# Kernel tuning notes

Measured on AMD Instinct MI355X. Metric: run time of the kernel, lower is better.

The kernel has to match this reference:

```python
import jax, jax.numpy as jnp
import numpy as np
from jax import lax

LEVEL_W = 512   # nodes per tree level (also = number of trees / batch_size)
DEPTH = 16      # tree depth
N = LEVEL_W * DEPTH
DIN = 512       # inputs_dim
H = 512         # hidden_dim
E = 200         # embed_dim (GloVe)
C = 150         # num classes


def setup_inputs() -> dict:
    key = jax.random.key(0)
    ks = jax.random.split(key, 8)
    features = jax.random.normal(ks[0], (N, DIN), jnp.float32)
    embed_table = jax.random.normal(ks[1], (C + 1, E), jnp.float32) * 0.1
    Wx = jax.random.normal(ks[2], (DIN + E, 4 * H), jnp.float32) / np.sqrt(DIN + E)
    Wh = jax.random.normal(ks[3], (H, 4 * H), jnp.float32) / np.sqrt(H)
    b = jnp.zeros((4 * H,), jnp.float32)
    out_W = jax.random.normal(ks[4], (H, C), jnp.float32) / np.sqrt(H)
    out_b = jnp.zeros((C,), jnp.float32)
    keep = 0.8  # dropout = 0.2 -> shared dropout mask, scaled by 1/keep
    dropout_mask = (jax.random.bernoulli(ks[5], keep, (H,)).astype(jnp.float32) / keep)
    # forest topology: level 0 nodes are roots (parent -1); level l node's parent
    # is a random node in level l-1 (parents always processed before children)
    rng = np.random.default_rng(0)
    parent = np.full((N,), -1, dtype=np.int32)
    for l in range(1, DEPTH):
        parent[l * LEVEL_W:(l + 1) * LEVEL_W] = rng.integers((l - 1) * LEVEL_W, l * LEVEL_W, LEVEL_W)
    order = rng.permutation(N).astype(np.int32)
    return {
        "features": features, "embed_table": embed_table,
        "Wx": Wx, "Wh": Wh, "b": b, "out_W": out_W, "out_b": out_b,
        "dropout_mask": dropout_mask,
        "parent_idx": jnp.asarray(parent), "order": jnp.asarray(order),
        "batch_size": LEVEL_W,
    }


def reference(features, embed_table, Wx, Wh, b, out_W, out_b, dropout_mask,
              parent_idx, order, batch_size):
    n, din = features.shape
    h_dim = Wh.shape[0]
    n_cls = out_W.shape[1]
    depth = n // LEVEL_W

    def cell(x, h, c):
        g = x @ Wx + h @ Wh + b
        i, f, gg, o = jnp.split(g, 4, axis=-1)
        c2 = jax.nn.sigmoid(f) * c + jax.nn.sigmoid(i) * jnp.tanh(gg)
        h2 = jax.nn.sigmoid(o) * jnp.tanh(c2)
        return h2, c2

    def step(carry, l):
        h_all, c_all, cm_all, d_all = carry
        off = l * LEVEL_W
        p = lax.dynamic_slice(parent_idx, (off,), (LEVEL_W,))
        root = p < 0
        pp = jnp.where(root, 0, p)
        h_par = jnp.where(root[:, None], 0.0, h_all[pp])
        c_par = jnp.where(root[:, None], 0.0, c_all[pp])
        # roots get the 'start' embedding (row 0); others embed parent's
        # committed (argmax) label shifted by 1
        eidx = jnp.where(root, 0, cm_all[pp] + 1)
        x = jnp.concatenate(
            [lax.dynamic_slice(features, (off, 0), (LEVEL_W, din)),
             embed_table[eidx]], axis=-1)
        h, c = cell(x, h_par, c_par)
        h = h * dropout_mask
        dist = h @ out_W + out_b
        cm = jnp.argmax(dist, axis=-1).astype(jnp.int32)
        carry = (lax.dynamic_update_slice(h_all, h, (off, 0)),
                 lax.dynamic_update_slice(c_all, c, (off, 0)),
                 lax.dynamic_update_slice(cm_all, cm, (off,)),
                 lax.dynamic_update_slice(d_all, dist, (off, 0)))
        return carry, None

    init = (jnp.zeros((n, h_dim), features.dtype),
            jnp.zeros((n, h_dim), features.dtype),
            jnp.zeros((n,), jnp.int32),
            jnp.zeros((n, n_cls), features.dtype))
    (h_all, c_all, cm_all, d_all), _ = lax.scan(step, init, jnp.arange(depth))
    # reorder from processing order back to node order, drop root entries
    out_dists = d_all[order][:-batch_size]
    out_commitments = cm_all[order][:-batch_size]
    return out_dists, out_commitments
```

## Files before the change

### kernel.cpp

```cpp
#include <hip/hip_runtime.h>
#include <math.h>

#define LEVEL_W 512
#define DEPTH   16
#define NNODES  8192
#define DIN     512
#define HD      512
#define ED      200
#define NC      150
#define GDIM    2048
#define OUTROWS 7680
#define KH      512
#define KW      1024
#define NKC     16

typedef __attribute__((ext_vector_type(8))) short s8v;
typedef __attribute__((ext_vector_type(4))) float f4v;

__device__ __forceinline__ unsigned short f2bf(float x) {
    unsigned int u = __float_as_uint(x);
    u += 0x7FFFu + ((u >> 16) & 1u);
    return (unsigned short)(u >> 16);
}
__device__ __forceinline__ float bf2f(unsigned short b) {
    return __uint_as_float(((unsigned int)b) << 16);
}
__device__ __forceinline__ float sigm(float x) { return 1.0f / (1.0f + expf(-x)); }

__device__ __forceinline__ void gl_lds16(const void* g, void* l) {
    __builtin_amdgcn_global_load_lds((const __attribute__((address_space(1))) void*)g,
                                     (__attribute__((address_space(3))) void*)l, 16, 0, 0);
}

__global__ __launch_bounds__(256) void prep_w(
    const float* __restrict__ Wx, const float* __restrict__ Wh,
    unsigned short* __restrict__ w_hi, unsigned short* __restrict__ w_lo)
{
    __shared__ float Wt[64][65];
    const int t   = threadIdx.x;
    const int b   = blockIdx.x;
    const int mat = b >> 5;
    const int ns  = b & 31;
    const float* src = mat ? Wx : Wh;

    for (int kw = 0; kw < 8; ++kw) {
        __syncthreads();
        #pragma unroll
        for (int p = 0; p < 16; ++p) {
            int gl  = p >> 2;
            int kk  = (p & 3) * 16 + (t >> 4);
            int col = gl * 512 + ns * 16 + (t & 15);
            Wt[kk][gl * 16 + (t & 15)] = src[(size_t)(kw * 64 + kk) * GDIM + col];
        }
        __syncthreads();
        {
            int nl  = t >> 2;
            int cp  = t & 3;
            int nsg = ns * 64 + nl;
            int key = nsg & 7;
            __align__(16) unsigned short hv[16], lv[16];
            #pragma unroll
            for (int e = 0; e < 16; ++e) {
                float x = Wt[cp * 16 + e][nl];
                unsigned short h = f2bf(x);
                hv[e] = h;
                lv[e] = f2bf(x - bf2f(h));
            }
            size_t base = (size_t)nsg * KW + mat * 512 + kw * 64;
            int c0 = cp * 2, c1 = cp * 2 + 1;
            *(uint4*)&w_hi[base + ((c0 ^ key) * 8)] = *(const uint4*)&hv[0];
            *(uint4*)&w_hi[base + ((c1 ^ key) * 8)] = *(const uint4*)&hv[8];
            *(uint4*)&w_lo[base + ((c0 ^ key) * 8)] = *(const uint4*)&lv[0];
            *(uint4*)&w_lo[base + ((c1 ^ key) * 8)] = *(const uint4*)&lv[8];
        }
    }
}

__global__ __launch_bounds__(256) void prep_feat(
    const float* __restrict__ features, const int* __restrict__ order,
    unsigned short* __restrict__ f_hi, unsigned short* __restrict__ f_lo,
    int* __restrict__ inv)
{
    int i = blockIdx.x * 256 + threadIdx.x;
    {
        int r  = i >> 5;
        int k0 = (i & 31) * 16;
        const float* srcp = features + (size_t)r * DIN + k0;
        __align__(16) unsigned short hv[16], lv[16];
        #pragma unroll
        for (int e = 0; e < 16; ++e) {
            float x = srcp[e];
            unsigned short h = f2bf(x);
            hv[e] = h;
            lv[e] = f2bf(x - bf2f(h));
        }
        int key = r & 7;
        int c0  = (k0 >> 3) & 7;
        size_t base = (size_t)r * KH + (k0 & ~63);
        *(uint4*)&f_hi[base + ((c0 ^ key) * 8)]       = *(const uint4*)&hv[0];
        *(uint4*)&f_hi[base + (((c0 + 1) ^ key) * 8)] = *(const uint4*)&hv[8];
        *(uint4*)&f_lo[base + ((c0 ^ key) * 8)]       = *(const uint4*)&lv[0];
        *(uint4*)&f_lo[base + (((c0 + 1) ^ key) * 8)] = *(const uint4*)&lv[8];
    }
    if (i < NNODES) inv[order[i]] = i;
}

__global__ __launch_bounds__(128) void prep_embed(
    const float* __restrict__ embed, const float* __restrict__ Wx,
    const float* __restrict__ bvec, float* __restrict__ g_embed)
{
    int e    = blockIdx.y;
    int np   = blockIdx.x * 128 + threadIdx.x;
    int gate = (np >> 4) & 3, hcs = np >> 6, hcl = np & 15;
    int col  = gate * 512 + hcs * 16 + hcl;
    float acc = bvec[col];
    const float* er = embed + (size_t)e * ED;
    for (int k = 0; k < ED; ++k)
        acc += er[k] * Wx[(size_t)(DIN + k) * GDIM + col];
    g_embed[(size_t)e * GDIM + np] = acc;
}

__global__ __launch_bounds__(128) void gemm_h_cell(
    float* h_all, float* c_all,
    const int* __restrict__ parent, const int* __restrict__ cm_all,
    const unsigned short* __restrict__ w_hi, const unsigned short* __restrict__ w_lo,
    const unsigned short* __restrict__ f_hi, const unsigned short* __restrict__ f_lo,
    const float* __restrict__ g_embed, const float* __restrict__ dropout, int off)
{
    __shared__ unsigned short Ah[32 * 64], Al[32 * 64], Bh[64 * 64], Bl[64 * 64];
    __shared__ int p_s[32], rt_s[32], ei_s[32];
    const int t = threadIdx.x, w = t >> 6, lane = t & 63;
    const int ns = blockIdx.x, mt = blockIdx.y;
    const int grow0 = off + mt * 32;

    if (t < 32) {
        int p  = parent[grow0 + t];
        int rt = (p < 0) ? 1 : 0;
        p_s[t]  = rt ? 0 : p;
        rt_s[t] = rt;
        ei_s[t] = rt ? 0 : (cm_all[rt ? 0 : p] + 1);
    }
    __syncthreads();

    f4v acc[4];
    #pragma unroll
    for (int i = 0; i < 4; ++i) acc[i] = (f4v){0.f, 0.f, 0.f, 0.f};

    const int ar  = t >> 2;
    const int aq  = t & 3;
    const int ap  = p_s[ar];
    const int art = rt_s[ar];
    const float* asrc = h_all + (size_t)ap * HD + aq * 16;
    const int akey = ar & 7;
    const int ac0  = aq * 2;

    for (int kc = 0; kc < NKC; ++kc) {
        if (kc < 8) {
            float x[16];
            if (art) {
                #pragma unroll
                for (int e = 0; e < 16; ++e) x[e] = 0.f;
            } else {
                const float4* s4 = (const float4*)(asrc + kc * 64);
                float4 v0 = s4[0], v1 = s4[1], v2 = s4[2], v3 = s4[3];
                x[0] = v0.x; x[1] = v0.y; x[2] = v0.z; x[3] = v0.w;
                x[4] = v1.x; x[5] = v1.y; x[6] = v1.z; x[7] = v1.w;
                x[8] = v2.x; x[9] = v2.y; x[10] = v2.z; x[11] = v2.w;
                x[12] = v3.x; x[13] = v3.y; x[14] = v3.z; x[15] = v3.w;
            }
            __align__(16) unsigned short hv[16], lv[16];
            #pragma unroll
            for (int e = 0; e < 16; ++e) {
                unsigned short h = f2bf(x[e]);
                hv[e] = h;
                lv[e] = f2bf(x[e] - bf2f(h));
            }
            *(uint4*)&Ah[ar * 64 + ((ac0 ^ akey) * 8)]       = *(const uint4*)&hv[0];
            *(uint4*)&Ah[ar * 64 + (((ac0 + 1) ^ akey) * 8)] = *(const uint4*)&hv[8];
            *(uint4*)&Al[ar * 64 + ((ac0 ^ akey) * 8)]       = *(const uint4*)&lv[0];
            *(uint4*)&Al[ar * 64 + (((ac0 + 1) ^ akey) * 8)] = *(const uint4*)&lv[8];
        } else {
            #pragma unroll
            for (int q = 0; q < 2; ++q) {
                int ia  = w * 2 + q;
                int row = ia * 8 + (lane >> 3);
                size_t aoff = ((size_t)(grow0 + row) * KH + (kc - 8) * 64) * 2
                              + (lane & 7) * 16;
                gl_lds16((const char*)f_hi + aoff, (char*)Ah + ia * 1024);
                gl_lds16((const char*)f_lo + aoff, (char*)Al + ia * 1024);
            }
        }
        #pragma unroll
        for (int q = 0; q < 4; ++q) {
            int ib  = w * 4 + q;
            int row = ib * 8 + (lane >> 3);
            size_t boff = ((size_t)(ns * 64 + row) * KW + kc * 64) * 2
                          + (lane & 7) * 16;
            gl_lds16((const char*)w_hi + boff, (char*)Bh + ib * 1024);
            gl_lds16((const char*)w_lo + boff, (char*)Bl + ib * 1024);
        }
        __syncthreads();
        #pragma unroll
        for (int s = 0; s < 2; ++s) {
            int arow = w * 16 + (lane & 15);
            int ach  = s * 4 + (lane >> 4);
            s8v ahv = *(const s8v*)&Ah[arow * 64 + ((ach ^ (arow & 7)) * 8)];
            s8v alv = *(const s8v*)&Al[arow * 64 + ((ach ^ (arow & 7)) * 8)];
            #pragma unroll
            for (int fn = 0; fn < 4; ++fn) {
                int brow = fn * 16 + (lane & 15);
                s8v bhv = *(const s8v*)&Bh[brow * 64 + ((ach ^ (brow & 7)) * 8)];
                s8v blv = *(const s8v*)&Bl[brow * 64 + ((ach ^ (brow & 7)) * 8)];
                acc[fn] = __builtin_amdgcn_mfma_f32_16x16x32_bf16(ahv, bhv, acc[fn], 0, 0, 0);
                acc[fn] = __builtin_amdgcn_mfma_f32_16x16x32_bf16(ahv, blv, acc[fn], 0, 0, 0);
                acc[fn] = __builtin_amdgcn_mfma_f32_16x16x32_bf16(alv, bhv, acc[fn], 0, 0, 0);
            }
        }
        __syncthreads();
    }

    const int hcl  = lane & 15;
    const int hcol = ns * 16 + hcl;
    const float dm = dropout[hcol];
    #pragma unroll
    for (int j = 0; j < 4; ++j) {
        int lr   = w * 16 + (lane >> 4) * 4 + j;
        int grow = grow0 + lr;
        const float* gep = g_embed + (size_t)ei_s[lr] * GDIM + ns * 64;
        float gi = acc[0][j] + gep[0 * 16 + hcl];
        float gf = acc[1][j] + gep[1 * 16 + hcl];
        float gg = acc[2][j] + gep[2 * 16 + hcl];
        float go = acc[3][j] + gep[3 * 16 + hcl];
        float cpar = rt_s[lr] ? 0.f : c_all[(size_t)p_s[lr] * HD + hcol];
        float c2 = sigm(gf) * cpar + sigm(gi) * tanhf(gg);
        float h2 = sigm(go) * tanhf(c2) * dm;
        c_all[(size_t)grow * HD + hcol] = c2;
        h_all[(size_t)grow * HD + hcol] = h2;
    }
}

__global__ __launch_bounds__(256) void level_dist(
    const float* __restrict__ h_all, const float* __restrict__ outW,
    const float* __restrict__ outb, const int* __restrict__ inv,
    float* __restrict__ d_out, int* __restrict__ cm_all, int off)
{
    __shared__ float h_s[4][512];
    __shared__ float dist_s[4][160];

    const int tid = threadIdx.x;
    const int r0  = blockIdx.x * 4;

    for (int i4 = tid; i4 < 512; i4 += 256) {
        int row = i4 >> 7;
        int k   = (i4 & 127) * 4;
        *(float4*)&h_s[row][k] =
            *(const float4*)&h_all[(size_t)(off + r0 + row) * HD + k];
    }
    __syncthreads();

    const int j = tid;
    if (j < NC) {
        float a0 = 0.f, a1 = 0.f, a2 = 0.f, a3 = 0.f;
        for (int k = 0; k < HD; ++k) {
            float w = outW[k * NC + j];
            a0 += h_s[0][k] * w;
            a1 += h_s[1][k] * w;
            a2 += h_s[2][k] * w;
            a3 += h_s[3][k] * w;
        }
        float bj = outb[j];
        dist_s[0][j] = a0 + bj;
        dist_s[1][j] = a1 + bj;
        dist_s[2][j] = a2 + bj;
        dist_s[3][j] = a3 + bj;
    }
    __syncthreads();

    if (j < NC) {
        #pragma unroll
        for (int r = 0; r < 4; ++r) {
            int orow = inv[off + r0 + r];
            if (orow < OUTROWS) d_out[(size_t)orow * NC + j] = dist_s[r][j];
        }
    }

    const int r    = tid >> 6;
    const int lane = tid & 63;
    float best = -3.402823466e38f;
    int   bidx = 0x7fffffff;
    for (int jj = lane; jj < NC; jj += 64) {
        float v = dist_s[r][jj];
        if (v > best || (v == best && jj < bidx)) { best = v; bidx = jj; }
    }
    #pragma unroll
    for (int m = 32; m >= 1; m >>= 1) {
        float ov = __shfl_xor(best, m);
        int   oi = __shfl_xor(bidx, m);
        if (ov > best || (ov == best && oi < bidx)) { best = ov; bidx = oi; }
    }
    if (lane == 0) {
        int grow = off + r0 + r;
        cm_all[grow] = bidx;
        int orow = inv[grow];
        if (orow < OUTROWS) d_out[(size_t)OUTROWS * NC + orow] = (float)bidx;
    }
}

extern "C" void kernel_launch(void* const* d_in, const int* in_sizes, int n_in,
                              void* d_out, int out_size, void* d_ws, size_t ws_size,
                              hipStream_t stream)
{
    const float* features = (const float*)d_in[0];
    const float* embed    = (const float*)d_in[1];
    const float* Wx       = (const float*)d_in[2];
    const float* Wh       = (const float*)d_in[3];
    const float* bias     = (const float*)d_in[4];
    const float* outW     = (const float*)d_in[5];
    const float* outb     = (const float*)d_in[6];
    const float* dropout  = (const float*)d_in[7];
    const int*   parent   = (const int*)d_in[8];
    const int*   order    = (const int*)d_in[9];

    char* p = (char*)d_ws;
    unsigned short* w_hi   = (unsigned short*)p; p += (size_t)GDIM * KW * 2;
    unsigned short* w_lo   = (unsigned short*)p; p += (size_t)GDIM * KW * 2;
    unsigned short* f_hi   = (unsigned short*)p; p += (size_t)NNODES * KH * 2;
    unsigned short* f_lo   = (unsigned short*)p; p += (size_t)NNODES * KH * 2;
    float*          g_emb  = (float*)p;          p += (size_t)(NC + 2) * GDIM * 4;
    float*          h_all  = (float*)p;          p += (size_t)NNODES * HD * 4;
    float*          c_all  = (float*)p;          p += (size_t)NNODES * HD * 4;
    int*            cm_all = (int*)p;            p += (size_t)NNODES * 4;
    int*            inv    = (int*)p;            p += (size_t)NNODES * 4;

    float* out = (float*)d_out;

    prep_w<<<64, 256, 0, stream>>>(Wx, Wh, w_hi, w_lo);
    prep_feat<<<1024, 256, 0, stream>>>(features, order, f_hi, f_lo, inv);
    prep_embed<<<dim3(16, NC + 1), 128, 0, stream>>>(embed, Wx, bias, g_emb);

    for (int l = 0; l < DEPTH; ++l) {
        int off = l * LEVEL_W;
        gemm_h_cell<<<dim3(32, 16), 128, 0, stream>>>(
            h_all, c_all, parent, cm_all, w_hi, w_lo, f_hi, f_lo, g_emb, dropout, off);
        level_dist<<<128, 256, 0, stream>>>(
            h_all, outW, outb, inv, out, cm_all, off);
    }
}
```

Measured before the change: 829.1 us.

## Fuse per-level GEMM and distribution kernels into one cooperative persistent kernel

Replaces the 32 per-level kernel launches with a single cooperative kernel of 512 blocks that loops over the 16 tree levels. Grid-wide syncs separate the gate GEMM plus LSTM cell phase from the per-node output projection and argmax phase. The aim is to remove launch overhead and inter-kernel gaps. In exchange, the output projection now runs with one block per node instead of the previous level_dist layout, and it depends on all 512 blocks being co-resident; if the cooperative launch fails, the code falls back to the old per-level kernels.

```diff
diff --git a/kernel.cpp b/kernel.cpp
--- a/kernel.cpp
+++ b/kernel.cpp
@@ -1,5 +1,9 @@
 #include <hip/hip_runtime.h>
+#include <hip/hip_cooperative_groups.h>
 #include <math.h>
+#include <float.h>
+
+namespace cg = cooperative_groups;
 
 #define LEVEL_W 512
 #define DEPTH   16
@@ -118,6 +122,192 @@
     for (int k = 0; k < ED; ++k)
         acc += er[k] * Wx[(size_t)(DIN + k) * GDIM + col];
     g_embed[(size_t)e * GDIM + np] = acc;
+}
+
+__global__ __launch_bounds__(128) void forest_kernel(
+    float* h_all, float* c_all,
+    const int* __restrict__ parent, int* __restrict__ cm_all,
+    const unsigned short* __restrict__ w_hi, const unsigned short* __restrict__ w_lo,
+    const unsigned short* __restrict__ f_hi, const unsigned short* __restrict__ f_lo,
+    const float* __restrict__ g_embed, const float* __restrict__ dropout,
+    const float* __restrict__ outW, const float* __restrict__ outb,
+    const int* __restrict__ inv, float* __restrict__ d_out)
+{
+    cg::grid_group grid = cg::this_grid();
+
+    __shared__ unsigned short Ah[32 * 64], Al[32 * 64], Bh[64 * 64], Bl[64 * 64];
+    __shared__ int p_s[32], rt_s[32], ei_s[32];
+    __shared__ float h_s[512];
+    __shared__ float dist_s[160];
+
+    const int t = threadIdx.x, w = t >> 6, lane = t & 63;
+    const int bid = blockIdx.x;
+    const int ns = bid & 31, mt = bid >> 5;
+
+    for (int l = 0; l < DEPTH; ++l) {
+        const int off = l * LEVEL_W;
+        {
+            const int grow0 = off + mt * 32;
+
+            if (t < 32) {
+                int p  = parent[grow0 + t];
+                int rt = (p < 0) ? 1 : 0;
+                p_s[t]  = rt ? 0 : p;
+                rt_s[t] = rt;
+                ei_s[t] = rt ? 0 : (cm_all[rt ? 0 : p] + 1);
+            }
+            __syncthreads();
+
+            f4v acc[4];
+            #pragma unroll
+            for (int i = 0; i < 4; ++i) acc[i] = (f4v){0.f, 0.f, 0.f, 0.f};
+
+            const int ar  = t >> 2;
+            const int aq  = t & 3;
+            const int ap  = p_s[ar];
+            const int art = rt_s[ar];
+            const float* asrc = h_all + (size_t)ap * HD + aq * 16;
+            const int akey = ar & 7;
+            const int ac0  = aq * 2;
+
+            for (int kc = 0; kc < NKC; ++kc) {
+                if (kc < 8) {
+                    float x[16];
+                    if (art) {
+                        #pragma unroll
+                        for (int e = 0; e < 16; ++e) x[e] = 0.f;
+                    } else {
+                        const float4* s4 = (const float4*)(asrc + kc * 64);
+                        float4 v0 = s4[0], v1 = s4[1], v2 = s4[2], v3 = s4[3];
+                        x[0] = v0.x; x[1] = v0.y; x[2] = v0.z; x[3] = v0.w;
+                        x[4] = v1.x; x[5] = v1.y; x[6] = v1.z; x[7] = v1.w;
+                        x[8] = v2.x; x[9] = v2.y; x[10] = v2.z; x[11] = v2.w;
+                        x[12] = v3.x; x[13] = v3.y; x[14] = v3.z; x[15] = v3.w;
+                    }
+                    __align__(16) unsigned short hv[16], lv[16];
+                    #pragma unroll
+                    for (int e = 0; e < 16; ++e) {
+                        unsigned short h = f2bf(x[e]);
+                        hv[e] = h;
+                        lv[e] = f2bf(x[e] - bf2f(h));
+                    }
+                    *(uint4*)&Ah[ar * 64 + ((ac0 ^ akey) * 8)]       = *(const uint4*)&hv[0];
+                    *(uint4*)&Ah[ar * 64 + (((ac0 + 1) ^ akey) * 8)] = *(const uint4*)&hv[8];
+                    *(uint4*)&Al[ar * 64 + ((ac0 ^ akey) * 8)]       = *(const uint4*)&lv[0];
+                    *(uint4*)&Al[ar * 64 + (((ac0 + 1) ^ akey) * 8)] = *(const uint4*)&lv[8];
+                } else {
+                    #pragma unroll
+                    for (int q = 0; q < 2; ++q) {
+                        int ia  = w * 2 + q;
+                        int row = ia * 8 + (lane >> 3);
+                        size_t aoff = ((size_t)(grow0 + row) * KH + (kc - 8) * 64) * 2
+                                      + (lane & 7) * 16;
+                        gl_lds16((const char*)f_hi + aoff, (char*)Ah + ia * 1024);
+                        gl_lds16((const char*)f_lo + aoff, (char*)Al + ia * 1024);
+                    }
+                }
+                #pragma unroll
+                for (int q = 0; q < 4; ++q) {
+                    int ib  = w * 4 + q;
+                    int row = ib * 8 + (lane >> 3);
+                    size_t boff = ((size_t)(ns * 64 + row) * KW + kc * 64) * 2
+                                  + (lane & 7) * 16;
+                    gl_lds16((const char*)w_hi + boff, (char*)Bh + ib * 1024);
+                    gl_lds16((const char*)w_lo + boff, (char*)Bl + ib * 1024);
+                }
+                __syncthreads();
+                #pragma unroll
+                for (int s = 0; s < 2; ++s) {
+                    int arow = w * 16 + (lane & 15);
+                    int ach  = s * 4 + (lane >> 4);
+                    s8v ahv = *(const s8v*)&Ah[arow * 64 + ((ach ^ (arow & 7)) * 8)];
+                    s8v alv = *(const s8v*)&Al[arow * 64 + ((ach ^ (arow & 7)) * 8)];
+                    #pragma unroll
+                    for (int fn = 0; fn < 4; ++fn) {
+                        int brow = fn * 16 + (lane & 15);
+                        s8v bhv = *(const s8v*)&Bh[brow * 64 + ((ach ^ (brow & 7)) * 8)];
+                        s8v blv = *(const s8v*)&Bl[brow * 64 + ((ach ^ (brow & 7)) * 8)];
+                        acc[fn] = __builtin_amdgcn_mfma_f32_16x16x32_bf16(ahv, bhv, acc[fn], 0, 0, 0);
+                        acc[fn] = __builtin_amdgcn_mfma_f32_16x16x32_bf16(ahv, blv, acc[fn], 0, 0, 0);
+                        acc[fn] = __builtin_amdgcn_mfma_f32_16x16x32_bf16(alv, bhv, acc[fn], 0, 0, 0);
+                    }
+                }
+                __syncthreads();
+            }
+
+            const int hcl  = lane & 15;
+            const int hcol = ns * 16 + hcl;
+            const float dm = dropout[hcol];
+            #pragma unroll
+            for (int j = 0; j < 4; ++j) {
+                int lr   = w * 16 + (lane >> 4) * 4 + j;
+                int grow = grow0 + lr;
+                const float* gep = g_embed + (size_t)ei_s[lr] * GDIM + ns * 64;
+                float gi = acc[0][j] + gep[0 * 16 + hcl];
+                float gf = acc[1][j] + gep[1 * 16 + hcl];
+                float gg = acc[2][j] + gep[2 * 16 + hcl];
+                float go = acc[3][j] + gep[3 * 16 + hcl];
+                float cpar = rt_s[lr] ? 0.f : c_all[(size_t)p_s[lr] * HD + hcol];
+                float c2 = sigm(gf) * cpar + sigm(gi) * tanhf(gg);
+                float h2 = sigm(go) * tanhf(c2) * dm;
+                c_all[(size_t)grow * HD + hcol] = c2;
+                h_all[(size_t)grow * HD + hcol] = h2;
+            }
+        }
+        __threadfence();
+        grid.sync();
+
+        {
+            const int grow = off + bid;
+            const float* hrow = h_all + (size_t)grow * HD;
+            *(float4*)&h_s[t * 4] = ((const float4*)hrow)[t];
+            __syncthreads();
+
+            const int j  = t;
+            const int j2 = t + 128;
+            if (j < NC) {
+                float a = 0.f;
+                #pragma unroll 8
+                for (int k = 0; k < HD; ++k) a += h_s[k] * outW[k * NC + j];
+                dist_s[j] = a + outb[j];
+            }
+            if (j2 < NC) {
+                float a = 0.f;
+                #pragma unroll 8
+                for (int k = 0; k < HD; ++k) a += h_s[k] * outW[k * NC + j2];
+                dist_s[j2] = a + outb[j2];
+            }
+            __syncthreads();
+
+            const int orow = inv[grow];
+            if (orow < OUTROWS) {
+                if (j < NC)  d_out[(size_t)orow * NC + j]  = dist_s[j];
+                if (j2 < NC) d_out[(size_t)orow * NC + j2] = dist_s[j2];
+            }
+
+            if (t < 64) {
+                float best = -FLT_MAX;
+                int   bidx = 0x7fffffff;
+                for (int jj = t; jj < NC; jj += 64) {
+                    float v = dist_s[jj];
+                    if (v > best || (v == best && jj < bidx)) { best = v; bidx = jj; }
+                }
+                #pragma unroll
+                for (int m = 32; m >= 1; m >>= 1) {
+                    float ov = __shfl_xor(best, m);
+                    int   oi = __shfl_xor(bidx, m);
+                    if (ov > best || (ov == best && oi < bidx)) { best = ov; bidx = oi; }
+                }
+                if (t == 0) {
+                    cm_all[grow] = bidx;
+                    if (orow < OUTROWS) d_out[(size_t)OUTROWS * NC + orow] = (float)bidx;
+                }
+            }
+            __syncthreads();
+        }
+        __threadfence();
+        grid.sync();
+    }
 }
 
 __global__ __launch_bounds__(128) void gemm_h_cell(
@@ -338,11 +528,22 @@
     prep_feat<<<1024, 256, 0, stream>>>(features, order, f_hi, f_lo, inv);
     prep_embed<<<dim3(16, NC + 1), 128, 0, stream>>>(embed, Wx, bias, g_emb);
 
-    for (int l = 0; l < DEPTH; ++l) {
-        int off = l * LEVEL_W;
-        gemm_h_cell<<<dim3(32, 16), 128, 0, stream>>>(
-            h_all, c_all, parent, cm_all, w_hi, w_lo, f_hi, f_lo, g_emb, dropout, off);
-        level_dist<<<128, 256, 0, stream>>>(
-            h_all, outW, outb, inv, out, cm_all, off);
-    }
-}
+    void* args[] = {
+        (void*)&h_all, (void*)&c_all, (void*)&parent, (void*)&cm_all,
+        (void*)&w_hi, (void*)&w_lo, (void*)&f_hi, (void*)&f_lo,
+        (void*)&g_emb, (void*)&dropout, (void*)&outW, (void*)&outb,
+        (void*)&inv, (void*)&out
+    };
+    hipError_t err = hipLaunchCooperativeKernel(
+        (const void*)forest_kernel, dim3(512), dim3(128), args, 0, stream);
+
+    if (err != hipSuccess) {
+        for (int l = 0; l < DEPTH; ++l) {
+            int off = l * LEVEL_W;
+            gemm_h_cell<<<dim3(32, 16), 128, 0, stream>>>(
+                h_all, c_all, parent, cm_all, w_hi, w_lo, f_hi, f_lo, g_emb, dropout, off);
+            level_dist<<<128, 256, 0, stream>>>(
+                h_all, outW, outb, inv, out, cm_all, off);
+        }
+    }
+}
```

After: 3.314 ms. 4x slower.
